# Optimization experiments

Measured on AMD Instinct MI355X. Metric: run time of the kernel, lower is better.

The kernel has to match this reference:

```python
import jax, jax.numpy as jnp
import numpy as np

jax.config.update("jax_enable_x64", True)

_FULL = 1 << 32
_MASK = _FULL - 1
_HALF = _FULL >> 1
_QUARTER = _HALF >> 1
_THREE_QUARTER = 3 * _QUARTER


def setup_inputs() -> dict:
    key = jax.random.key(0)
    num_symbols = 262144            # e.g. a 512x512 plane of {-1,+1} symbols
    num_bits = 2 * num_symbols      # compressed payload, ~2 bits/symbol budget
    payload_bits = jax.random.randint(key, (num_bits,), 0, 2, dtype=jnp.int64)
    return {
        "payload_bits": payload_bits,
        "total_freq": 4096,         # 1 << frequency_precision (12)
        "num_symbols": num_symbols,
        "context_bits": 8,
    }


def reference(payload_bits, total_freq, num_symbols, context_bits):
    bits = payload_bits.astype(jnp.int64)
    nb = bits.shape[0]
    num_states = 1 << context_bits
    smask = num_states - 1

    def read_bit(ptr):
        # _BitReader returns 0 past the end of the payload
        return jnp.where(ptr < nb, bits[jnp.clip(ptr, 0, nb - 1)], jnp.int64(0))

    # initial 32-bit code word
    idx32 = jnp.arange(32, dtype=jnp.int64)
    b32 = jnp.where(idx32 < nb, bits[jnp.clip(idx32, 0, nb - 1)], 0)
    code0 = jnp.sum(b32 << (31 - idx32))

    def renorm(carry):
        # E1/E2/E3 renormalization loop (bit-level, data dependent)
        def cond(c):
            low, high, code, ptr = c
            return (high < _HALF) | (low >= _HALF) | ((low >= _QUARTER) & (high < _THREE_QUARTER))

        def body(c):
            low, high, code, ptr = c
            sub = jnp.where(high < _HALF, jnp.int64(0),
                            jnp.where(low >= _HALF, jnp.int64(_HALF), jnp.int64(_QUARTER)))
            low = low - sub
            high = high - sub
            code = code - sub
            low = (low << 1) & _MASK
            high = ((high << 1) & _MASK) | 1
            code = ((code << 1) & _MASK) | read_bit(ptr)
            return (low, high, code, ptr + 1)

        return jax.lax.while_loop(cond, body, carry)

    def step(carry, _):
        low, high, code, ptr, state, count0, count1 = carry
        n0 = count0[state]
        n1 = count1[state]
        total = n0 + n1
        p0 = n0.astype(jnp.float64) / total.astype(jnp.float64)
        p0_freq = jnp.clip(jnp.rint(p0 * (total_freq - 2)) + 1.0, 1.0, float(total_freq - 1)).astype(jnp.int64)
        rng = high - low + 1                      # fits int64 (<= 2^32)
        scaled = ((code - low + 1) * total_freq - 1) // rng
        split = low + rng * p0_freq // total_freq
        bit = (scaled >= p0_freq).astype(jnp.int64)
        low2 = jnp.where(bit == 0, low, split)
        high2 = jnp.where(bit == 0, split - 1, high)
        low3, high3, code3, ptr3 = renorm((low2, high2, code, ptr))
        count0 = count0.at[state].add(1 - bit)
        count1 = count1.at[state].add(bit)
        state2 = ((state << 1) | bit) & smask
        return (low3, high3, code3, ptr3, state2, count0, count1), bit

    init = (
        jnp.int64(0),               # low
        jnp.int64(_MASK),           # high = 2^32 - 1
        code0.astype(jnp.int64),    # code
        jnp.int64(32),              # bit pointer (32 bits consumed)
        jnp.int64(0),               # context state
        jnp.ones(num_states, dtype=jnp.int64),  # count0 (Laplace init)
        jnp.ones(num_states, dtype=jnp.int64),  # count1
    )
    _, out_bits = jax.lax.scan(step, init, None, length=num_symbols)
    # map {0,1} -> {-1,+1} float32 symbols (reshape to bitstream.shape is metadata-only)
    return out_bits.astype(jnp.float32) * 2.0 - 1.0
```

## Files before the change

kernel.cpp:

```cpp
#include <hip/hip_runtime.h>


#define WORDS_LDS 16400
#define MAX_STATES 1024

__device__ __forceinline__ long long ddiv_floor(long long n, long long d) {
    double qd = (double)n / (double)d;
    long long q = (long long)qd;
    long long r = n - q * d;
    q -= (r < 0);
    q += (r >= d);
    return q;
}

template<bool POW2>
__device__ __forceinline__ void decode_serial(
    const unsigned* __restrict__ words, int4* __restrict__ tab,
    const int* __restrict__ bits, int nb,
    long long total_freq, int tf_shift, int num_symbols, int smask,
    float* __restrict__ out)
{
    const unsigned long long M = 0xFFFFFFFFull;
    const unsigned long long H = 0x80000000ull;
    const double tfm2d = (double)(total_freq - 2);
    const int tfm1 = (int)(total_freq - 1);

    unsigned long long low = 0, high = M;
    unsigned long long code = words[0];
    unsigned long long bitbuf = (((unsigned long long)words[1]) << 32) | words[2];
    int navail = 64;
    unsigned pre = words[3];
    int widx = 4;

    int state = 0;
    int4 c = tab[0];
    int n0 = c.x, n1 = c.y, pf = c.z;

    for (int s = 0; s < num_symbols; ++s) {
        int c0 = (state << 1) & smask;
        int4 q0 = tab[c0];
        int4 q1 = tab[c0 | 1];

        if (navail <= 32) {
            bitbuf |= ((unsigned long long)pre) << (32 - navail);
            navail += 32;
            unsigned nxt;
            if (widx < WORDS_LDS) {
                nxt = words[widx];
            } else {
                unsigned g = 0;
                long long base = ((long long)widx) << 5;
                for (int j = 0; j < 32; ++j) {
                    long long idx = base + j;
                    int bb = (idx < nb) ? (bits[idx] & 1) : 0;
                    g |= ((unsigned)bb) << (31 - j);
                }
                nxt = g;
            }
            pre = nxt;
            ++widx;
        }

        unsigned long long rng = high - low + 1;
        unsigned long long P = (unsigned long long)(unsigned)pf * rng;
        unsigned long long dlt = code - low + 1;
        unsigned long long N = POW2 ? ((dlt << tf_shift) - 1ull)
                                    : (dlt * (unsigned long long)total_freq - 1ull);
        int bit = (N >= P) ? 1 : 0;
        unsigned long long soff = POW2 ? (P >> tf_shift)
                                       : (unsigned long long)ddiv_floor((long long)P, total_freq);
        unsigned long long split = low + soff;
        low  = bit ? split : low;
        high = bit ? high : (split - 1ull);
        out[s] = bit ? 1.0f : -1.0f;

        int nn0 = n0 + 1 - bit;
        int nn1 = n1 + bit;
        double p0d = (double)nn0 / (double)(nn0 + nn1);
        double pfd = rint(p0d * tfm2d) + 1.0;
        int pfn = (int)pfd;
        pfn = pfn < 1 ? 1 : pfn;
        pfn = pfn > tfm1 ? tfm1 : pfn;

        unsigned x = (unsigned)(low ^ high);
        int k = __builtin_clzll((((unsigned long long)x) << 32) | 1ull);
        k = k > 32 ? 32 : k;
        low  = (low << k) & M;
        high = ((high << k) | ((1ull << k) - 1ull)) & M;
        unsigned long long tk = (bitbuf >> (63 - k)) >> 1;
        code = ((code << k) & M) | tk;
        bitbuf <<= k;
        navail -= k;
        unsigned l32 = (unsigned)low, h32 = (unsigned)high;
        int a = __builtin_clz(~(l32 << 1));
        int b = __builtin_clz((h32 << 1) | 1u);
        int m = a < b ? a : b;
        unsigned long long ones = (1ull << m) - 1ull;
        low  = ((low << m) - ones * H) & M;
        high = ((high << m) - ones * (H - 1ull)) & M;
        unsigned long long tm = (bitbuf >> (63 - m)) >> 1;
        code = ((code << m) - ones * H + tm) & M;
        bitbuf <<= m;
        navail -= m;

        tab[state] = make_int4(nn0, nn1, pfn, 0);

        int nidx = c0 | bit;
        int4 q;
        q.x = bit ? q1.x : q0.x;
        q.y = bit ? q1.y : q0.y;
        q.z = bit ? q1.z : q0.z;
        if (nidx == state) { q.x = nn0; q.y = nn1; q.z = pfn; }
        state = nidx;
        n0 = q.x; n1 = q.y; pf = q.z;
    }
}

__global__ __launch_bounds__(256)
void EntropyDecoder_84928683311460_kernel(
    const int* __restrict__ bits,
    const int* __restrict__ tf_p,
    const int* __restrict__ ns_p,
    const int* __restrict__ cb_p,
    float* __restrict__ out,
    int nb)
{
    __shared__ unsigned words[WORDS_LDS];
    __shared__ int4 tab[MAX_STATES];

    const int tid = threadIdx.x;
    const long long total_freq = (long long)(*tf_p);
    const int num_symbols = *ns_p;
    const int context_bits = *cb_p;
    const int num_states = 1 << context_bits;
    const int smask = num_states - 1;

    for (int w = tid; w < WORDS_LDS; w += blockDim.x) {
        unsigned v = 0;
        int base = w << 5;
        if (base + 32 <= nb) {
            #pragma unroll
            for (int j = 0; j < 32; j += 4) {
                int4 b4 = *reinterpret_cast<const int4*>(bits + base + j);
                v |= ((unsigned)(b4.x & 1) << (31 - j))
                   | ((unsigned)(b4.y & 1) << (30 - j))
                   | ((unsigned)(b4.z & 1) << (29 - j))
                   | ((unsigned)(b4.w & 1) << (28 - j));
            }
        } else if (base < nb) {
            for (int j = 0; j < 32; ++j) {
                int idx = base + j;
                int b = (idx < nb) ? (bits[idx] & 1) : 0;
                v |= ((unsigned)b) << (31 - j);
            }
        }
        words[w] = v;
    }
    {
        double p0d = 0.5;
        double pfd = rint(p0d * (double)(total_freq - 2)) + 1.0;
        int pf0 = (int)pfd;
        int tfm1 = (int)(total_freq - 1);
        pf0 = pf0 < 1 ? 1 : (pf0 > tfm1 ? tfm1 : pf0);
        for (int st = tid; st < num_states; st += blockDim.x)
            tab[st] = make_int4(1, 1, pf0, 0);
    }
    __syncthreads();
    if (tid != 0) return;

    int tf_shift = 31 - __builtin_clz((unsigned)total_freq);
    if ((total_freq & (total_freq - 1)) == 0)
        decode_serial<true >(words, tab, bits, nb, total_freq, tf_shift, num_symbols, smask, out);
    else
        decode_serial<false>(words, tab, bits, nb, total_freq, tf_shift, num_symbols, smask, out);
}

extern "C" void kernel_launch(void* const* d_in, const int* in_sizes, int n_in,
                              void* d_out, int out_size, void* d_ws, size_t ws_size,
                              hipStream_t stream) {
    const int* bits = (const int*)d_in[0];
    const int* tf   = (const int*)d_in[1];
    const int* ns   = (const int*)d_in[2];
    const int* cb   = (const int*)d_in[3];
    float* out = (float*)d_out;
    int nb = in_sizes[0];

    hipLaunchKernelGGL(EntropyDecoder_84928683311460_kernel,
                       dim3(1), dim3(256), 0, stream,
                       bits, tf, ns, cb, out, nb);
}
```

Before: 87.07 ms.

## Narrow decoder state to 32-bit, pack context table, defer table writeback

Rewrites the serial arithmetic-decoder loop so low, high and code are held in 32-bit registers, and folds the two renormalization phases into a single combined shift. The per-state counts are packed into two 32-bit words, so one 16-byte LDS load fetches both candidate next states. The table write is delayed by one symbol through a forwarding register, taking the LDS store off the critical dependency chain. This is meant to shorten the latency of each serial step. In exchange it packs count1 into 20 bits, which could overflow on very skewed inputs, and adds forwarding logic that must stay correct.

After: 81.13 ms. 6.8% less time.

```diff
diff --git a/kernel.cpp b/kernel.cpp
--- a/kernel.cpp
+++ b/kernel.cpp
@@ -15,45 +15,47 @@
 
 template<bool POW2>
 __device__ __forceinline__ void decode_serial(
-    const unsigned* __restrict__ words, int4* __restrict__ tab,
-    const int* __restrict__ bits, int nb,
-    long long total_freq, int tf_shift, int num_symbols, int smask,
-    float* __restrict__ out)
+    const unsigned* __restrict__ words, unsigned* tab,
+    const int* __restrict__ bits, int nb, int nwords,
+    unsigned total_freq, int tf_shift, int num_symbols, int smask,
+    unsigned pf0, float* __restrict__ out)
 {
-    const unsigned long long M = 0xFFFFFFFFull;
-    const unsigned long long H = 0x80000000ull;
-    const double tfm2d = (double)(total_freq - 2);
-    const int tfm1 = (int)(total_freq - 1);
-
-    unsigned long long low = 0, high = M;
-    unsigned long long code = words[0];
-    unsigned long long bitbuf = (((unsigned long long)words[1]) << 32) | words[2];
+    const unsigned H = 0x80000000u;
+    unsigned low = 0u, high = 0xFFFFFFFFu;
+    unsigned code = words[0];
+    unsigned long long bitbuf = (((unsigned long long)words[1]) << 32) | (unsigned long long)words[2];
     int navail = 64;
     unsigned pre = words[3];
     int widx = 4;
 
+    const double tfm2d = (double)(total_freq - 2u);
+    const int tfm1 = (int)(total_freq - 1u);
+
     int state = 0;
-    int4 c = tab[0];
-    int n0 = c.x, n1 = c.y, pf = c.z;
+    unsigned n0 = 1u, n1 = 1u, pf = pf0;
+
+    int wIdx = 0;
+    unsigned wN0 = 1u, wN1 = 1u, wPf = pf0;
+
+    float* op = out;
 
     for (int s = 0; s < num_symbols; ++s) {
-        int c0 = (state << 1) & smask;
-        int4 q0 = tab[c0];
-        int4 q1 = tab[c0 | 1];
+        const int c0 = (state << 1) & smask;
+        uint4 q = *reinterpret_cast<const uint4*>(tab + 2 * c0);
 
         if (navail <= 32) {
             bitbuf |= ((unsigned long long)pre) << (32 - navail);
             navail += 32;
-            unsigned nxt;
+            unsigned nxt = 0u;
             if (widx < WORDS_LDS) {
                 nxt = words[widx];
-            } else {
-                unsigned g = 0;
+            } else if (widx < nwords) {
+                unsigned g = 0u;
                 long long base = ((long long)widx) << 5;
                 for (int j = 0; j < 32; ++j) {
                     long long idx = base + j;
-                    int bb = (idx < nb) ? (bits[idx] & 1) : 0;
-                    g |= ((unsigned)bb) << (31 - j);
+                    int b = (idx < (long long)nb) ? (bits[idx] & 1) : 0;
+                    g |= ((unsigned)b) << (31 - j);
                 }
                 nxt = g;
             }
@@ -61,58 +63,64 @@
             ++widx;
         }
 
-        unsigned long long rng = high - low + 1;
-        unsigned long long P = (unsigned long long)(unsigned)pf * rng;
-        unsigned long long dlt = code - low + 1;
-        unsigned long long N = POW2 ? ((dlt << tf_shift) - 1ull)
-                                    : (dlt * (unsigned long long)total_freq - 1ull);
-        int bit = (N >= P) ? 1 : 0;
-        unsigned long long soff = POW2 ? (P >> tf_shift)
-                                       : (unsigned long long)ddiv_floor((long long)P, total_freq);
-        unsigned long long split = low + soff;
+        const unsigned rngm1 = high - low;
+        const unsigned long long P = (unsigned long long)pf * rngm1 + pf;
+        const unsigned dlt = code - low;
+        const unsigned long long N = POW2
+            ? ((((unsigned long long)dlt) << tf_shift) + (unsigned long long)tfm1)
+            : ((unsigned long long)dlt * total_freq + (unsigned long long)(total_freq - 1u));
+        const int bit = (N >= P) ? 1 : 0;
+        const unsigned soff = POW2 ? (unsigned)(P >> tf_shift)
+                                   : (unsigned)ddiv_floor((long long)P, (long long)total_freq);
+        const unsigned split = low + soff;
         low  = bit ? split : low;
-        high = bit ? high : (split - 1ull);
-        out[s] = bit ? 1.0f : -1.0f;
-
-        int nn0 = n0 + 1 - bit;
-        int nn1 = n1 + bit;
-        double p0d = (double)nn0 / (double)(nn0 + nn1);
+        high = bit ? high : (split - 1u);
+        *op++ = bit ? 1.0f : -1.0f;
+
+        const unsigned nn0 = n0 + (unsigned)(1 - bit);
+        const unsigned nn1 = n1 + (unsigned)bit;
+        double p0d = (double)(int)nn0 / (double)(int)(nn0 + nn1);
         double pfd = rint(p0d * tfm2d) + 1.0;
-        int pfn = (int)pfd;
-        pfn = pfn < 1 ? 1 : pfn;
-        pfn = pfn > tfm1 ? tfm1 : pfn;
-
-        unsigned x = (unsigned)(low ^ high);
-        int k = __builtin_clzll((((unsigned long long)x) << 32) | 1ull);
-        k = k > 32 ? 32 : k;
-        low  = (low << k) & M;
-        high = ((high << k) | ((1ull << k) - 1ull)) & M;
-        unsigned long long tk = (bitbuf >> (63 - k)) >> 1;
-        code = ((code << k) & M) | tk;
-        bitbuf <<= k;
-        navail -= k;
-        unsigned l32 = (unsigned)low, h32 = (unsigned)high;
-        int a = __builtin_clz(~(l32 << 1));
-        int b = __builtin_clz((h32 << 1) | 1u);
-        int m = a < b ? a : b;
-        unsigned long long ones = (1ull << m) - 1ull;
-        low  = ((low << m) - ones * H) & M;
-        high = ((high << m) - ones * (H - 1ull)) & M;
-        unsigned long long tm = (bitbuf >> (63 - m)) >> 1;
-        code = ((code << m) - ones * H + tm) & M;
-        bitbuf <<= m;
-        navail -= m;
-
-        tab[state] = make_int4(nn0, nn1, pfn, 0);
-
-        int nidx = c0 | bit;
-        int4 q;
-        q.x = bit ? q1.x : q0.x;
-        q.y = bit ? q1.y : q0.y;
-        q.z = bit ? q1.z : q0.z;
-        if (nidx == state) { q.x = nn0; q.y = nn1; q.z = pfn; }
+        int pfi = (int)pfd;
+        pfi = pfi < 1 ? 1 : (pfi > tfm1 ? tfm1 : pfi);
+        const unsigned pfn = (unsigned)pfi;
+
+        const unsigned x = low ^ high;
+        const int k = __builtin_clz(x);
+        const unsigned aa = ~(low << (k + 1));
+        const unsigned bb = (high << (k + 1)) | ((2u << k) - 1u);
+        const int ca = __builtin_clz(aa);
+        const int cb = __builtin_clz(bb);
+        const int m = ca < cb ? ca : cb;
+        const int K = k + m;
+        const unsigned sub = (m != 0) ? H : 0u;
+        const unsigned ones = (1u << K) - 1u;
+        const unsigned t13 = (unsigned)(bitbuf >> 51);
+        const unsigned tK = t13 >> (13 - K);
+        low  = (low << K) - sub;
+        high = (high << K) + ones - sub;
+        code = ((code << K) | tK) - sub;
+        bitbuf <<= K;
+        navail -= K;
+
+        const int nidx = c0 | bit;
+        const unsigned sw0 = bit ? q.z : q.x;
+        const unsigned sw1 = bit ? q.w : q.y;
+        const bool f2 = (nidx == wIdx);
+        unsigned xn0 = f2 ? wN0 : sw0;
+        unsigned xn1 = f2 ? wN1 : (sw1 & 0xFFFFFu);
+        unsigned xpf = f2 ? wPf : (sw1 >> 20);
+
+        *reinterpret_cast<uint2*>(tab + 2 * wIdx) = make_uint2(wN0, wN1 | (wPf << 20));
+
+        wIdx = state; wN0 = nn0; wN1 = nn1; wPf = pfn;
+
+        if (__builtin_expect(nidx == state, 0)) {
+            asm volatile("");
+            xn0 = nn0; xn1 = nn1; xpf = pfn;
+        }
         state = nidx;
-        n0 = q.x; n1 = q.y; pf = q.z;
+        n0 = xn0; n1 = xn1; pf = xpf;
     }
 }
 
@@ -126,14 +134,15 @@
     int nb)
 {
     __shared__ unsigned words[WORDS_LDS];
-    __shared__ int4 tab[MAX_STATES];
+    __shared__ __align__(16) unsigned tab[MAX_STATES * 2];
 
     const int tid = threadIdx.x;
-    const long long total_freq = (long long)(*tf_p);
+    const unsigned total_freq = (unsigned)(*tf_p);
     const int num_symbols = *ns_p;
     const int context_bits = *cb_p;
     const int num_states = 1 << context_bits;
     const int smask = num_states - 1;
+    const int nwords = (nb + 31) >> 5;
 
     for (int w = tid; w < WORDS_LDS; w += blockDim.x) {
         unsigned v = 0;
@@ -156,23 +165,28 @@
         }
         words[w] = v;
     }
+    unsigned pf0;
     {
-        double p0d = 0.5;
-        double pfd = rint(p0d * (double)(total_freq - 2)) + 1.0;
-        int pf0 = (int)pfd;
-        int tfm1 = (int)(total_freq - 1);
-        pf0 = pf0 < 1 ? 1 : (pf0 > tfm1 ? tfm1 : pf0);
-        for (int st = tid; st < num_states; st += blockDim.x)
-            tab[st] = make_int4(1, 1, pf0, 0);
+        double pfd = rint(0.5 * (double)(total_freq - 2u)) + 1.0;
+        int t = (int)pfd;
+        int tfm1 = (int)(total_freq - 1u);
+        t = t < 1 ? 1 : (t > tfm1 ? tfm1 : t);
+        pf0 = (unsigned)t;
+    }
+    for (int st = tid; st < num_states; st += blockDim.x) {
+        tab[2 * st]     = 1u;
+        tab[2 * st + 1] = 1u | (pf0 << 20);
     }
     __syncthreads();
     if (tid != 0) return;
 
-    int tf_shift = 31 - __builtin_clz((unsigned)total_freq);
-    if ((total_freq & (total_freq - 1)) == 0)
-        decode_serial<true >(words, tab, bits, nb, total_freq, tf_shift, num_symbols, smask, out);
+    const int tf_shift = 31 - __builtin_clz(total_freq);
+    if ((total_freq & (total_freq - 1u)) == 0u)
+        decode_serial<true >(words, tab, bits, nb, nwords, total_freq, tf_shift,
+                             num_symbols, smask, pf0, out);
     else
-        decode_serial<false>(words, tab, bits, nb, total_freq, tf_shift, num_symbols, smask, out);
+        decode_serial<false>(words, tab, bits, nb, nwords, total_freq, tf_shift,
+                             num_symbols, smask, pf0, out);
 }
 
 extern "C" void kernel_launch(void* const* d_in, const int* in_sizes, int n_in,
```
